# Optimization experiments

Hardware: AMD Instinct MI355X
Metric: run time of the kernel (lower is better)

## Reference

```python
import jax, jax.numpy as jnp
import numpy as np

EPS = 1e-5

def mean_std_norm(x):
    # instance norm without affine: per-(B,C) mean/std over spatial dims
    mean = jnp.mean(x, axis=(2, 3), keepdims=True)
    var = jnp.var(x, axis=(2, 3), keepdims=True)
    return (x - mean) / jnp.sqrt(var + EPS)

def conv1x1(x, w, b):
    # x: [B,C,H,W], w: [O,C], b: [O]
    return jnp.einsum('oc,bchw->bohw', w, x) + b[None, :, None, None]

def setup_inputs() -> dict:
    key = jax.random.key(0)
    ks = jax.random.split(key, 9)
    C = 512
    s = 1.0 / np.sqrt(C)
    inp = {
        'content_feat': jax.random.normal(ks[0], (4, C, 64, 64), dtype=jnp.float32),
        'f_w': jax.random.normal(ks[1], (C, C), dtype=jnp.float32) * s,
        'f_b': jnp.zeros((C,), dtype=jnp.float32),
        'g_w': jax.random.normal(ks[2], (C, C), dtype=jnp.float32) * s,
        'g_b': jnp.zeros((C,), dtype=jnp.float32),
        'h_w': jax.random.normal(ks[3], (C, C), dtype=jnp.float32) * s,
        'h_b': jnp.zeros((C,), dtype=jnp.float32),
        'o_w': jax.random.normal(ks[4], (C, C), dtype=jnp.float32) * s,
        'o_b': jnp.zeros((C,), dtype=jnp.float32),
    }
    return inp

def reference(content_feat, f_w, f_b, g_w, g_b, h_w, h_b, o_w, o_b):
    B, C, H, W = content_feat.shape
    HW = H * W
    norm = mean_std_norm(content_feat)
    # f(norm) -> [B, HW, C]; g(norm) -> [B, C, HW]
    F_Fc = conv1x1(norm, f_w, f_b).reshape(B, C, HW).transpose(0, 2, 1)
    G_Fs = conv1x1(norm, g_w, g_b).reshape(B, C, HW)
    energy = jnp.einsum('bnc,bcm->bnm', F_Fc, G_Fs)  # [B, HW, HW]
    attention = jax.nn.softmax(energy, axis=-1)
    H_Fs = conv1x1(content_feat, h_w, h_b).reshape(B, C, HW)
    # out = H_Fs @ attention^T : out[b,c,m] = sum_n H_Fs[b,c,n] * att[b,m,n]
    out = jnp.einsum('bcn,bmn->bcm', H_Fs, attention).reshape(B, C, H, W)
    out = conv1x1(out, o_w, o_b)
    return out + content_feat
```

## Files before the change

### kernel.cpp

```cpp
#include <hip/hip_runtime.h>


typedef __bf16 bf16_t;
typedef _Float16 f16_t;
typedef _Float16 f16x8 __attribute__((ext_vector_type(8)));
typedef float f32x4 __attribute__((ext_vector_type(4)));

#define LOG2E 1.44269504088896340736f

__device__ __forceinline__ void gload16(const void* g, void* l) {
  __builtin_amdgcn_global_load_lds(
      (const __attribute__((address_space(1))) void*)g,
      (__attribute__((address_space(3))) void*)l, 16, 0, 0);
}

__global__ void __launch_bounds__(256) stats_k(const float* __restrict__ x,
                                               float* __restrict__ mu,
                                               float* __restrict__ rs,
                                               f16_t* __restrict__ xv) {
  const int bc = blockIdx.x;
  const float4* row = (const float4*)(x + (size_t)bc * 4096);
  f16_t* vrow = xv + (size_t)bc * 4096;
  float s = 0.f, ss = 0.f;
  for (int i = threadIdx.x; i < 1024; i += 256) {
    float4 v = row[i];
    s += v.x + v.y + v.z + v.w;
    ss += v.x * v.x + v.y * v.y + v.z * v.z + v.w * v.w;
    alignas(8) f16_t h[4];
    h[0] = (f16_t)v.x; h[1] = (f16_t)v.y; h[2] = (f16_t)v.z; h[3] = (f16_t)v.w;
    *(uint2*)(vrow + i * 4) = *(const uint2*)h;
  }
#pragma unroll
  for (int o = 32; o >= 1; o >>= 1) {
    s += __shfl_down(s, o);
    ss += __shfl_down(ss, o);
  }
  __shared__ float as_[4], ass_[4];
  const int w = threadIdx.x >> 6;
  if ((threadIdx.x & 63) == 0) { as_[w] = s; ass_[w] = ss; }
  __syncthreads();
  if (threadIdx.x == 0) {
    float st = as_[0] + as_[1] + as_[2] + as_[3];
    float sst = ass_[0] + ass_[1] + ass_[2] + ass_[3];
    float m = st * (1.f / 4096.f);
    float var = sst * (1.f / 4096.f) - m * m;
    mu[bc] = m;
    rs[bc] = rsqrtf(var + 1e-5f);
  }
}

__global__ void __launch_bounds__(256) mt_k(const float* __restrict__ fw,
                                            const float* __restrict__ gw,
                                            f16_t* __restrict__ Mh) {
  __shared__ float Fs[32][64];
  __shared__ float Gs[32][64];
  const int t = threadIdx.x;
  const int it = blockIdx.x, jt = blockIdx.y;
  float acc[16];
#pragma unroll
  for (int i = 0; i < 16; ++i) acc[i] = 0.f;
  const int jl = t >> 2, ib = (t & 3) * 16;
  const int lr = t >> 4, lc4 = (t & 15) * 4;
  for (int cc = 0; cc < 16; ++cc) {
    __syncthreads();
#pragma unroll
    for (int rep = 0; rep < 2; ++rep) {
      const int r = lr + rep * 16;
      *(float4*)&Fs[r][lc4] = *(const float4*)(fw + (size_t)(cc * 32 + r) * 512 + it * 64 + lc4);
      *(float4*)&Gs[r][lc4] = *(const float4*)(gw + (size_t)(cc * 32 + r) * 512 + jt * 64 + lc4);
    }
    __syncthreads();
#pragma unroll
    for (int c = 0; c < 32; ++c) {
      const float gv = Gs[c][jl];
#pragma unroll
      for (int ii = 0; ii < 16; ++ii) acc[ii] += gv * Fs[c][ib + ii];
    }
  }
  alignas(16) f16_t hi[16];
#pragma unroll
  for (int ii = 0; ii < 16; ++ii) hi[ii] = (f16_t)acc[ii];
  const size_t o = (size_t)(jt * 64 + jl) * 512 + it * 64 + ib;
  *(uint4*)(Mh + o) = *(const uint4*)hi;
  *(uint4*)(Mh + o + 8) = *(const uint4*)(hi + 8);
}

__global__ void __launch_bounds__(256) mt2_k(const float* __restrict__ hw,
                                             const float* __restrict__ ow,
                                             f16_t* __restrict__ Wf) {
  __shared__ float Fs[32][64];
  __shared__ float Os[64][33];
  const int t = threadIdx.x;
  const int it = blockIdx.x, jt = blockIdx.y;
  float acc[16];
#pragma unroll
  for (int i = 0; i < 16; ++i) acc[i] = 0.f;
  const int jl = t >> 2, ib = (t & 3) * 16;
  const int lr = t >> 4, lc4 = (t & 15) * 4;
  const int oj = t >> 2, ok = (t & 3) * 8;
  for (int kc = 0; kc < 16; ++kc) {
    __syncthreads();
#pragma unroll
    for (int rep = 0; rep < 2; ++rep) {
      const int r = lr + rep * 16;
      *(float4*)&Fs[r][lc4] = *(const float4*)(hw + (size_t)(kc * 32 + r) * 512 + it * 64 + lc4);
    }
    {
      const float4 a = *(const float4*)(ow + (size_t)(jt * 64 + oj) * 512 + kc * 32 + ok);
      const float4 bq = *(const float4*)(ow + (size_t)(jt * 64 + oj) * 512 + kc * 32 + ok + 4);
      Os[oj][ok] = a.x; Os[oj][ok + 1] = a.y; Os[oj][ok + 2] = a.z; Os[oj][ok + 3] = a.w;
      Os[oj][ok + 4] = bq.x; Os[oj][ok + 5] = bq.y; Os[oj][ok + 6] = bq.z; Os[oj][ok + 7] = bq.w;
    }
    __syncthreads();
#pragma unroll
    for (int k = 0; k < 32; ++k) {
      const float gv = Os[jl][k];
#pragma unroll
      for (int ii = 0; ii < 16; ++ii) acc[ii] += gv * Fs[k][ib + ii];
    }
  }
  alignas(16) f16_t hi[16];
#pragma unroll
  for (int ii = 0; ii < 16; ++ii) hi[ii] = (f16_t)acc[ii];
  const size_t o = (size_t)(jt * 64 + jl) * 512 + it * 64 + ib;
  *(uint4*)(Wf + o) = *(const uint4*)hi;
  *(uint4*)(Wf + o + 8) = *(const uint4*)(hi + 8);
}

__global__ void __launch_bounds__(256) v_k(const float* __restrict__ gw,
                                           const float* __restrict__ fb,
                                           float* __restrict__ v) {
  const int j = blockIdx.x * 256 + threadIdx.x;
  float s = 0.f;
  for (int c = 0; c < 512; ++c) s += gw[(size_t)c * 512 + j] * fb[c];
  v[j] = s;
}

__global__ void __launch_bounds__(256) bias2_k(const float* __restrict__ ow,
                                               const float* __restrict__ hb,
                                               const float* __restrict__ ob,
                                               float* __restrict__ b2) {
  const int w = threadIdx.x >> 6, lane = threadIdx.x & 63;
  const int j = blockIdx.x * 4 + w;
  const float4 a = *(const float4*)(ow + (size_t)j * 512 + lane * 8);
  const float4 b = *(const float4*)(ow + (size_t)j * 512 + lane * 8 + 4);
  const float4 h0 = *(const float4*)(hb + lane * 8);
  const float4 h1 = *(const float4*)(hb + lane * 8 + 4);
  float s = a.x * h0.x + a.y * h0.y + a.z * h0.z + a.w * h0.w +
            b.x * h1.x + b.y * h1.y + b.z * h1.z + b.w * h1.w;
#pragma unroll
  for (int o2 = 32; o2 >= 1; o2 >>= 1) s += __shfl_down(s, o2);
  if (lane == 0) b2[j] = s + ob[j];
}

__global__ void __launch_bounds__(256) u_k(const float* __restrict__ v,
                                           const f16_t* __restrict__ xf,
                                           float* __restrict__ u) {
  const int w = threadIdx.x >> 6, lane = threadIdx.x & 63;
  const int m = blockIdx.x * 4 + w;
  const int b = blockIdx.y;
  const size_t o = ((size_t)b * 4096 + m) * 512 + lane * 8;
  const f16x8 vh = *(const f16x8*)(xf + o);
  const float4 v0 = *(const float4*)(v + lane * 8);
  const float4 v1 = *(const float4*)(v + lane * 8 + 4);
  float s = 0.f;
  const float* vp = &v0.x;
#pragma unroll
  for (int e = 0; e < 4; ++e) s += (float)vh[e] * vp[e];
  const float* vq = &v1.x;
#pragma unroll
  for (int e = 0; e < 4; ++e) s += (float)vh[4 + e] * vq[e];
#pragma unroll
  for (int o2 = 32; o2 >= 1; o2 >>= 1) s += __shfl_down(s, o2);
  if (lane == 0) u[(size_t)b * 4096 + m] = s;
}

__global__ void __launch_bounds__(256) normt_k(const float* __restrict__ x,
                                               const float* __restrict__ mu,
                                               const float* __restrict__ rs,
                                               f16_t* __restrict__ xf) {
  __shared__ float tile[64][65];
  const int t = threadIdx.x;
  const int nt = blockIdx.x, ct = blockIdx.y, b = blockIdx.z;
  const float* src = x + ((size_t)b * 512 + ct * 64) * 4096 + nt * 64;
  {
    const int r = t >> 4, cq = (t & 15) * 4;
#pragma unroll
    for (int it = 0; it < 4; ++it) {
      const int rr = r + it * 16;
      const float4 v = *(const float4*)(src + (size_t)rr * 4096 + cq);
      tile[rr][cq] = v.x; tile[rr][cq + 1] = v.y;
      tile[rr][cq + 2] = v.z; tile[rr][cq + 3] = v.w;
    }
  }
  __syncthreads();
  const int n = t & 63, ch = t >> 6;
  alignas(16) f16_t vf[16];
#pragma unroll
  for (int i = 0; i < 16; ++i) {
    const int c = ch * 16 + i;
    const float v = tile[c][n];
    const int gc = b * 512 + ct * 64 + c;
    vf[i] = (f16_t)((v - mu[gc]) * rs[gc]);
  }
  const size_t o = ((size_t)b * 4096 + nt * 64 + n) * 512 + ct * 64 + ch * 16;
  *(uint4*)(xf + o) = *(const uint4*)vf;
  *(uint4*)(xf + o + 8) = *(const uint4*)(vf + 8);
}

template <typename OT, int BIAS, bool RESID>
__global__ void __launch_bounds__(256) gemm_k(const f16_t* __restrict__ A,
                                              const f16_t* __restrict__ Bt,
                                              OT* __restrict__ C,
                                              const float* __restrict__ biasM,
                                              const float* __restrict__ biasN,
                                              const float* __restrict__ resid,
                                              long sAb, long sBb, long sCb, int ldC) {
  __shared__ alignas(16) f16_t As[2][128 * 64];
  __shared__ alignas(16) f16_t Bs[2][128 * 64];
  const int t = threadIdx.x;
  const int lane = t & 63;
  const int w = t >> 6;
  const int wr = w >> 1, wc = w & 1;
  const int l15 = lane & 15, lg = lane >> 4;
  const int b = blockIdx.z;
  const int m0 = blockIdx.y * 128, n0 = blockIdx.x * 128;
  const f16_t* Ab = A + (size_t)sAb * b + (size_t)m0 * 512;
  const f16_t* Bb = Bt + (size_t)sBb * b + (size_t)n0 * 512;
  const int srow = t >> 3;
  const int slot = t & 7;

  auto gstage = [&](int pb_, int ks_) {
#pragma unroll
    for (int r_ = 0; r_ < 4; ++r_) {
      const int rr_ = r_ * 32 + srow;
      const size_t go_ = (size_t)rr_ * 512 + ks_ * 64 + ((slot ^ (rr_ & 7)) * 8);
      gload16(Ab + go_, (char*)As[pb_] + r_ * 4096 + w * 1024);
      gload16(Bb + go_, (char*)Bs[pb_] + r_ * 4096 + w * 1024);
    }
  };

  const f32x4 z4 = {0.f, 0.f, 0.f, 0.f};
  f32x4 acc[4][4];
#pragma unroll
  for (int i = 0; i < 4; ++i)
#pragma unroll
    for (int j = 0; j < 4; ++j) acc[i][j] = z4;

  gstage(0, 0);
  __syncthreads();
  for (int ks = 0; ks < 8; ++ks) {
    const int pb = ks & 1;
    if (ks < 7) gstage(pb ^ 1, ks + 1);
#pragma unroll
    for (int kk = 0; kk < 2; ++kk) {
      f16x8 af[4], bfr[4];
#pragma unroll
      for (int i = 0; i < 4; ++i) {
        const int ra = wr * 64 + i * 16 + l15;
        af[i] = *(const f16x8*)((const char*)As[pb] + ra * 128 + (((kk * 4 + lg) ^ (ra & 7)) * 16));
        const int rb = wc * 64 + i * 16 + l15;
        bfr[i] = *(const f16x8*)((const char*)Bs[pb] + rb * 128 + (((kk * 4 + lg) ^ (rb & 7)) * 16));
      }
#pragma unroll
      for (int i = 0; i < 4; ++i)
#pragma unroll
        for (int j = 0; j < 4; ++j)
          acc[i][j] = __builtin_amdgcn_mfma_f32_16x16x32_f16(af[i], bfr[j], acc[i][j], 0, 0, 0);
    }
    __syncthreads();
  }
  OT* Cb = C + (size_t)sCb * b;
#pragma unroll
  for (int i = 0; i < 4; ++i) {
#pragma unroll
    for (int j = 0; j < 4; ++j) {
      const int n = n0 + wc * 64 + j * 16 + l15;
      float bn = 0.f;
      if (BIAS == 2) bn = biasN[n];
#pragma unroll
      for (int r = 0; r < 4; ++r) {
        const int m = m0 + wr * 64 + i * 16 + lg * 4 + r;
        float v = acc[i][j][r] + bn;
        if (BIAS == 1) v += biasM[m];
        if (RESID) v += resid[(size_t)sCb * b + (size_t)m * ldC + n];
        Cb[(size_t)m * ldC + n] = (OT)v;
      }
    }
  }
}

__global__ void __launch_bounds__(512, 1) flash_k(const f16_t* __restrict__ Z,
                                                  const f16_t* __restrict__ X,
                                                  const float* __restrict__ u,
                                                  const f16_t* __restrict__ Hv,
                                                  f16_t* __restrict__ Oat_t) {
  __shared__ alignas(16) f16_t K[2][64 * 256];
  __shared__ alignas(16) f16_t P[64 * 72];
  __shared__ float redm[4][2][16];
  __shared__ float reds[4][2][16];
  __shared__ float alds[64];
  __shared__ float llds[64];

  const int t = threadIdx.x;
  const int lane = t & 63;
  const int w = t >> 6;
  const int wq = w & 3, wk = w >> 2;
  const int l15 = lane & 15, lg = lane >> 4;
  const int bid = blockIdx.x;
  const int xcd = bid & 7;
  const int b = xcd >> 1;
  const int q0 = ((xcd & 1) * 32 + (bid >> 3)) * 64;

  const f16_t* Kb = X + (size_t)b * 4096 * 512;
  const f16_t* Vb = Hv + (size_t)b * 512 * 4096;
  const float* ub = u + (size_t)b * 4096;

  const int srow = w * 2 + (lane >> 5);
  const int slot32 = lane & 31;

  auto stagek = [&](int pb_, int kt_, int hf_) {
    const int k0_ = kt_ * 64;
#pragma unroll
    for (int r_ = 0; r_ < 4; ++r_) {
      const int row_ = r_ * 16 + srow;
      const size_t go_ = (size_t)(k0_ + row_) * 512 + hf_ * 256 + ((slot32 ^ (row_ & 7)) * 8);
      gload16(Kb + go_, (char*)K[pb_] + r_ * 8192 + w * 1024);
    }
  };

#define QKHALF(PB, HF)                                                                        \
  do {                                                                                        \
    _Pragma("unroll") for (int cwl_ = 0; cwl_ < 8; ++cwl_) {                                  \
      const f16x8 qf_ = qf[(HF) * 8 + cwl_];                                                  \
      _Pragma("unroll") for (int mf_ = 0; mf_ < 2; ++mf_) {                                   \
        const int key_ = 32 * wk + 16 * mf_ + l15;                                            \
        const int so_ = ((cwl_ * 4 + lg) ^ (key_ & 7)) * 16;                                  \
        const f16x8 kf_ = *(const f16x8*)((const char*)K[PB] + key_ * 512 + so_);             \
        sacc[mf_] = __builtin_amdgcn_mfma_f32_16x16x32_f16(kf_, qf_, sacc[mf_], 0, 0, 0);     \
      }                                                                                       \
    }                                                                                         \
  } while (0)

  f16x8 qf[16];
  {
    const size_t qo = ((size_t)b * 4096 + q0 + 16 * wq + l15) * 512 + lg * 8;
#pragma unroll
    for (int cw = 0; cw < 16; ++cw) qf[cw] = *(const f16x8*)(Z + qo + cw * 32);
  }
  stagek(0, 0, 0);

  const f32x4 z4 = {0.f, 0.f, 0.f, 0.f};
  f32x4 oacc[4][4];
#pragma unroll
  for (int i = 0; i < 4; ++i)
#pragma unroll
    for (int j = 0; j < 4; ++j) oacc[i][j] = z4;
  float m_run = -3.0e38f, l_run = 0.f;
  const int qrow = 16 * wq + l15;

  __syncthreads();

  for (int kt = 0; kt < 64; ++kt) {
    const int k0 = kt * 64;
    f32x4 sacc[2] = {z4, z4};
    const float4 u0 = *(const float4*)(ub + k0 + 32 * wk + 4 * lg);
    const float4 u1 = *(const float4*)(ub + k0 + 32 * wk + 16 + 4 * lg);
    stagek(1, kt, 1);
    QKHALF(0, 0);
    __syncthreads();
    if (kt < 63) stagek(0, kt + 1, 0);
    f16x8 vpre[4][2];
#pragma unroll
    for (int ct = 0; ct < 4; ++ct) {
      const int c = 64 * w + 16 * ct + l15;
#pragma unroll
      for (int kk = 0; kk < 2; ++kk)
        vpre[ct][kk] = *(const f16x8*)(Vb + (size_t)c * 4096 + k0 + kk * 32 + lg * 8);
    }
    QKHALF(1, 1);
    float pm = -3.0e38f;
    {
      const float* up0 = &u0.x;
      const float* up1 = &u1.x;
#pragma unroll
      for (int j = 0; j < 4; ++j) {
        sacc[0][j] += up0[j];
        sacc[1][j] += up1[j];
        pm = fmaxf(pm, fmaxf(sacc[0][j], sacc[1][j]));
      }
    }
    pm = fmaxf(pm, __shfl_xor(pm, 16));
    pm = fmaxf(pm, __shfl_xor(pm, 32));
    if (lane < 16) redm[wq][wk][lane] = pm;
    __syncthreads();
    const float m_tile = fmaxf(pm, redm[wq][wk ^ 1][l15]);
    float alpha;
    if (m_tile > m_run + 8.f) {
      alpha = exp2f((m_run - m_tile) * LOG2E);
      m_run = m_tile;
    } else {
      alpha = 1.f;
    }
    float ps = 0.f;
    {
      alignas(8) f16_t pk[4];
#pragma unroll
      for (int mf = 0; mf < 2; ++mf) {
#pragma unroll
        for (int j = 0; j < 4; ++j) {
          const float p = exp2f((sacc[mf][j] - m_run) * LOG2E);
          ps += p;
          pk[j] = (f16_t)p;
        }
        *(uint2*)((char*)P + qrow * 144 + 64 * wk + 32 * mf + 8 * lg) = *(const uint2*)pk;
      }
    }
    ps += __shfl_xor(ps, 16);
    ps += __shfl_xor(ps, 32);
    if (lane < 16) {
      reds[wq][wk][lane] = ps;
      if (wk == 0) alds[16 * wq + lane] = alpha;
    }
    __syncthreads();
    const float s_tile = reds[wq][0][l15] + reds[wq][1][l15];
    l_run = l_run * alpha + s_tile;
    float aq[4];
#pragma unroll
    for (int qt = 0; qt < 4; ++qt) aq[qt] = alds[16 * qt + l15];
    const bool need = (aq[0] != 1.f) || (aq[1] != 1.f) || (aq[2] != 1.f) || (aq[3] != 1.f);
    if (__any(need)) {
#pragma unroll
      for (int ct = 0; ct < 4; ++ct)
#pragma unroll
        for (int qt = 0; qt < 4; ++qt) oacc[ct][qt] *= aq[qt];
    }
#pragma unroll
    for (int kk = 0; kk < 2; ++kk) {
      f16x8 bp[4];
#pragma unroll
      for (int qt = 0; qt < 4; ++qt) {
        const int q = 16 * qt + l15;
        bp[qt] = *(const f16x8*)((const char*)P + q * 144 + kk * 64 + lg * 16);
      }
#pragma unroll
      for (int ct = 0; ct < 4; ++ct)
#pragma unroll
        for (int qt = 0; qt < 4; ++qt)
          oacc[ct][qt] =
              __builtin_amdgcn_mfma_f32_16x16x32_f16(vpre[ct][kk], bp[qt], oacc[ct][qt], 0, 0, 0);
    }
  }
#undef QKHALF
  if (wk == 0 && lane < 16) llds[16 * wq + lane] = l_run;
  __syncthreads();
  float inv[4];
#pragma unroll
  for (int qt = 0; qt < 4; ++qt) inv[qt] = 1.f / llds[16 * qt + l15];
#pragma unroll
  for (int ct = 0; ct < 4; ++ct)
#pragma unroll
    for (int qt = 0; qt < 4; ++qt) {
      alignas(8) f16_t o4[4];
#pragma unroll
      for (int j = 0; j < 4; ++j) o4[j] = (f16_t)(oacc[ct][qt][j] * inv[qt]);
      *(uint2*)(Oat_t + ((size_t)b * 4096 + q0 + 16 * qt + l15) * 512 + 64 * w + 16 * ct + 4 * lg) =
          *(const uint2*)o4;
    }
}

extern "C" void kernel_launch(void* const* d_in, const int* in_sizes, int n_in,
                              void* d_out, int out_size, void* d_ws, size_t ws_size,
                              hipStream_t stream) {
  const float* x = (const float*)d_in[0];
  const float* fw = (const float*)d_in[1];
  const float* fb = (const float*)d_in[2];
  const float* gw = (const float*)d_in[3];
  const float* gb = (const float*)d_in[4];
  const float* hw = (const float*)d_in[5];
  const float* hb = (const float*)d_in[6];
  const float* ow = (const float*)d_in[7];
  const float* ob = (const float*)d_in[8];
  float* out = (float*)d_out;
  (void)gb;

  const size_t BIG = (size_t)4 * 4096 * 512 * sizeof(f16_t);
  char* p = (char*)d_ws;
  float* mu = (float*)p; p += 2048 * sizeof(float);
  float* rs = (float*)p; p += 2048 * sizeof(float);
  float* vv = (float*)p; p += 512 * sizeof(float);
  float* b2 = (float*)p; p += 512 * sizeof(float);
  float* uu = (float*)p; p += (size_t)4 * 4096 * sizeof(float);
  f16_t* Mh = (f16_t*)p; p += (size_t)512 * 512 * sizeof(f16_t);
  f16_t* Wf = (f16_t*)p; p += (size_t)512 * 512 * sizeof(f16_t);
  f16_t* xf = (f16_t*)p; p += BIG;
  f16_t* xv = (f16_t*)p; p += BIG;
  f16_t* Zf = (f16_t*)p; p += BIG;
  f16_t* Oat_t = (f16_t*)p; p += BIG;

  const long sD = (long)4096 * 512;

  stats_k<<<2048, 256, 0, stream>>>(x, mu, rs, xv);
  mt_k<<<dim3(8, 8), 256, 0, stream>>>(fw, gw, Mh);
  mt2_k<<<dim3(8, 8), 256, 0, stream>>>(hw, ow, Wf);
  v_k<<<2, 256, 0, stream>>>(gw, fb, vv);
  bias2_k<<<128, 256, 0, stream>>>(ow, hb, ob, b2);
  normt_k<<<dim3(64, 8, 4), 256, 0, stream>>>(x, mu, rs, xf);
  u_k<<<dim3(1024, 4), 256, 0, stream>>>(vv, xf, uu);
  gemm_k<f16_t, 0, false><<<dim3(4, 32, 4), 256, 0, stream>>>(
      xf, Mh, Zf, nullptr, nullptr, nullptr, sD, 0, sD, 512);
  flash_k<<<256, 512, 0, stream>>>(Zf, xf, uu, xv, Oat_t);
  gemm_k<float, 1, true><<<dim3(32, 4, 4), 256, 0, stream>>>(
      Wf, Oat_t, out, b2, nullptr, x, 0, sD, sD, 4096);

  (void)in_sizes; (void)n_in; (void)out_size; (void)ws_size;
}
```

Measured before the change: 389.7 us.

## Merge weight-prep kernels into one launch and split QK MFMA accumulator chains

Four small weight-preprocessing kernels (two weight products and two bias vectors) are combined into a single launch, with blocks dispatching by index, to cut launch overhead. The bias2 computation changes from a wave-per-row shuffle reduction to a serial per-thread loop over strided rows. Separately, the QK score loop in the flash kernel now alternates between two independent accumulator sets per key fragment to shorten MFMA dependency chains. The extra accumulators raise register pressure in the flash kernel.

```diff
diff --git a/kernel.cpp b/kernel.cpp
--- a/kernel.cpp
+++ b/kernel.cpp
@@ -49,13 +49,11 @@
   }
 }
 
-__global__ void __launch_bounds__(256) mt_k(const float* __restrict__ fw,
-                                            const float* __restrict__ gw,
-                                            f16_t* __restrict__ Mh) {
-  __shared__ float Fs[32][64];
-  __shared__ float Gs[32][64];
+__device__ void mt_body(const float* __restrict__ A, const float* __restrict__ B,
+                        f16_t* __restrict__ Out, int it, int jt, float* sm, bool bIsJK) {
+  float* Fs = sm;
+  float* Gs = sm + 2048;
   const int t = threadIdx.x;
-  const int it = blockIdx.x, jt = blockIdx.y;
   float acc[16];
 #pragma unroll
   for (int i = 0; i < 16; ++i) acc[i] = 0.f;
@@ -66,91 +64,63 @@
 #pragma unroll
     for (int rep = 0; rep < 2; ++rep) {
       const int r = lr + rep * 16;
-      *(float4*)&Fs[r][lc4] = *(const float4*)(fw + (size_t)(cc * 32 + r) * 512 + it * 64 + lc4);
-      *(float4*)&Gs[r][lc4] = *(const float4*)(gw + (size_t)(cc * 32 + r) * 512 + jt * 64 + lc4);
+      *(float4*)&Fs[r * 64 + lc4] = *(const float4*)(A + (size_t)(cc * 32 + r) * 512 + it * 64 + lc4);
+      if (!bIsJK)
+        *(float4*)&Gs[r * 64 + lc4] = *(const float4*)(B + (size_t)(cc * 32 + r) * 512 + jt * 64 + lc4);
+    }
+    if (bIsJK) {
+      const int oj = t >> 2, ok = (t & 3) * 8;
+      const float4 a = *(const float4*)(B + (size_t)(jt * 64 + oj) * 512 + cc * 32 + ok);
+      const float4 bq = *(const float4*)(B + (size_t)(jt * 64 + oj) * 512 + cc * 32 + ok + 4);
+      Gs[oj * 33 + ok] = a.x; Gs[oj * 33 + ok + 1] = a.y;
+      Gs[oj * 33 + ok + 2] = a.z; Gs[oj * 33 + ok + 3] = a.w;
+      Gs[oj * 33 + ok + 4] = bq.x; Gs[oj * 33 + ok + 5] = bq.y;
+      Gs[oj * 33 + ok + 6] = bq.z; Gs[oj * 33 + ok + 7] = bq.w;
     }
     __syncthreads();
 #pragma unroll
     for (int c = 0; c < 32; ++c) {
-      const float gv = Gs[c][jl];
-#pragma unroll
-      for (int ii = 0; ii < 16; ++ii) acc[ii] += gv * Fs[c][ib + ii];
+      const float gv = bIsJK ? Gs[jl * 33 + c] : Gs[c * 64 + jl];
+#pragma unroll
+      for (int ii = 0; ii < 16; ++ii) acc[ii] += gv * Fs[c * 64 + ib + ii];
     }
   }
   alignas(16) f16_t hi[16];
 #pragma unroll
   for (int ii = 0; ii < 16; ++ii) hi[ii] = (f16_t)acc[ii];
   const size_t o = (size_t)(jt * 64 + jl) * 512 + it * 64 + ib;
-  *(uint4*)(Mh + o) = *(const uint4*)hi;
-  *(uint4*)(Mh + o + 8) = *(const uint4*)(hi + 8);
-}
-
-__global__ void __launch_bounds__(256) mt2_k(const float* __restrict__ hw,
-                                             const float* __restrict__ ow,
-                                             f16_t* __restrict__ Wf) {
-  __shared__ float Fs[32][64];
-  __shared__ float Os[64][33];
-  const int t = threadIdx.x;
-  const int it = blockIdx.x, jt = blockIdx.y;
-  float acc[16];
-#pragma unroll
-  for (int i = 0; i < 16; ++i) acc[i] = 0.f;
-  const int jl = t >> 2, ib = (t & 3) * 16;
-  const int lr = t >> 4, lc4 = (t & 15) * 4;
-  const int oj = t >> 2, ok = (t & 3) * 8;
-  for (int kc = 0; kc < 16; ++kc) {
-    __syncthreads();
-#pragma unroll
-    for (int rep = 0; rep < 2; ++rep) {
-      const int r = lr + rep * 16;
-      *(float4*)&Fs[r][lc4] = *(const float4*)(hw + (size_t)(kc * 32 + r) * 512 + it * 64 + lc4);
-    }
-    {
-      const float4 a = *(const float4*)(ow + (size_t)(jt * 64 + oj) * 512 + kc * 32 + ok);
-      const float4 bq = *(const float4*)(ow + (size_t)(jt * 64 + oj) * 512 + kc * 32 + ok + 4);
-      Os[oj][ok] = a.x; Os[oj][ok + 1] = a.y; Os[oj][ok + 2] = a.z; Os[oj][ok + 3] = a.w;
-      Os[oj][ok + 4] = bq.x; Os[oj][ok + 5] = bq.y; Os[oj][ok + 6] = bq.z; Os[oj][ok + 7] = bq.w;
-    }
-    __syncthreads();
-#pragma unroll
-    for (int k = 0; k < 32; ++k) {
-      const float gv = Os[jl][k];
-#pragma unroll
-      for (int ii = 0; ii < 16; ++ii) acc[ii] += gv * Fs[k][ib + ii];
-    }
-  }
-  alignas(16) f16_t hi[16];
-#pragma unroll
-  for (int ii = 0; ii < 16; ++ii) hi[ii] = (f16_t)acc[ii];
-  const size_t o = (size_t)(jt * 64 + jl) * 512 + it * 64 + ib;
-  *(uint4*)(Wf + o) = *(const uint4*)hi;
-  *(uint4*)(Wf + o + 8) = *(const uint4*)(hi + 8);
-}
-
-__global__ void __launch_bounds__(256) v_k(const float* __restrict__ gw,
-                                           const float* __restrict__ fb,
-                                           float* __restrict__ v) {
-  const int j = blockIdx.x * 256 + threadIdx.x;
-  float s = 0.f;
-  for (int c = 0; c < 512; ++c) s += gw[(size_t)c * 512 + j] * fb[c];
-  v[j] = s;
-}
-
-__global__ void __launch_bounds__(256) bias2_k(const float* __restrict__ ow,
-                                               const float* __restrict__ hb,
-                                               const float* __restrict__ ob,
-                                               float* __restrict__ b2) {
-  const int w = threadIdx.x >> 6, lane = threadIdx.x & 63;
-  const int j = blockIdx.x * 4 + w;
-  const float4 a = *(const float4*)(ow + (size_t)j * 512 + lane * 8);
-  const float4 b = *(const float4*)(ow + (size_t)j * 512 + lane * 8 + 4);
-  const float4 h0 = *(const float4*)(hb + lane * 8);
-  const float4 h1 = *(const float4*)(hb + lane * 8 + 4);
-  float s = a.x * h0.x + a.y * h0.y + a.z * h0.z + a.w * h0.w +
-            b.x * h1.x + b.y * h1.y + b.z * h1.z + b.w * h1.w;
-#pragma unroll
-  for (int o2 = 32; o2 >= 1; o2 >>= 1) s += __shfl_down(s, o2);
-  if (lane == 0) b2[j] = s + ob[j];
+  *(uint4*)(Out + o) = *(const uint4*)hi;
+  *(uint4*)(Out + o + 8) = *(const uint4*)(hi + 8);
+}
+
+__global__ void __launch_bounds__(256) prep_k(const float* __restrict__ fw,
+                                              const float* __restrict__ gw,
+                                              const float* __restrict__ hw,
+                                              const float* __restrict__ ow,
+                                              const float* __restrict__ fb,
+                                              const float* __restrict__ hb,
+                                              const float* __restrict__ ob,
+                                              f16_t* __restrict__ Mh,
+                                              f16_t* __restrict__ Wf,
+                                              float* __restrict__ vv,
+                                              float* __restrict__ b2) {
+  __shared__ float sm[2048 + 64 * 33];
+  const int bb = blockIdx.x;
+  if (bb < 64) {
+    mt_body(fw, gw, Mh, bb & 7, bb >> 3, sm, false);
+  } else if (bb < 128) {
+    mt_body(hw, ow, Wf, (bb - 64) & 7, (bb - 64) >> 3, sm, true);
+  } else if (bb < 130) {
+    const int j = (bb - 128) * 256 + threadIdx.x;
+    float s = 0.f;
+    for (int c = 0; c < 512; ++c) s += gw[(size_t)c * 512 + j] * fb[c];
+    vv[j] = s;
+  } else {
+    const int j = (bb - 130) * 256 + threadIdx.x;
+    float s = 0.f;
+    for (int c = 0; c < 512; ++c) s += ow[(size_t)j * 512 + c] * hb[c];
+    b2[j] = s + ob[j];
+  }
 }
 
 __global__ void __launch_bounds__(256) u_k(const float* __restrict__ v,
@@ -331,15 +301,25 @@
 
 #define QKHALF(PB, HF)                                                                        \
   do {                                                                                        \
+    f32x4 e0 = z4, e1 = z4, d0 = z4, d1 = z4;                                                 \
     _Pragma("unroll") for (int cwl_ = 0; cwl_ < 8; ++cwl_) {                                  \
       const f16x8 qf_ = qf[(HF) * 8 + cwl_];                                                  \
-      _Pragma("unroll") for (int mf_ = 0; mf_ < 2; ++mf_) {                                   \
-        const int key_ = 32 * wk + 16 * mf_ + l15;                                            \
-        const int so_ = ((cwl_ * 4 + lg) ^ (key_ & 7)) * 16;                                  \
-        const f16x8 kf_ = *(const f16x8*)((const char*)K[PB] + key_ * 512 + so_);             \
-        sacc[mf_] = __builtin_amdgcn_mfma_f32_16x16x32_f16(kf_, qf_, sacc[mf_], 0, 0, 0);     \
+      const int key0_ = 32 * wk + l15;                                                        \
+      const int key1_ = 32 * wk + 16 + l15;                                                   \
+      const f16x8 kf0_ = *(const f16x8*)((const char*)K[PB] + key0_ * 512 +                   \
+                                         (((cwl_ * 4 + lg) ^ (key0_ & 7)) * 16));             \
+      const f16x8 kf1_ = *(const f16x8*)((const char*)K[PB] + key1_ * 512 +                   \
+                                         (((cwl_ * 4 + lg) ^ (key1_ & 7)) * 16));             \
+      if (cwl_ & 1) {                                                                         \
+        d0 = __builtin_amdgcn_mfma_f32_16x16x32_f16(kf0_, qf_, d0, 0, 0, 0);                  \
+        d1 = __builtin_amdgcn_mfma_f32_16x16x32_f16(kf1_, qf_, d1, 0, 0, 0);                  \
+      } else {                                                                                \
+        e0 = __builtin_amdgcn_mfma_f32_16x16x32_f16(kf0_, qf_, e0, 0, 0, 0);                  \
+        e1 = __builtin_amdgcn_mfma_f32_16x16x32_f16(kf1_, qf_, e1, 0, 0, 0);                  \
       }                                                                                       \
     }                                                                                         \
+    sacc[0] += e0 + d0;                                                                       \
+    sacc[1] += e1 + d1;                                                                       \
   } while (0)
 
   f16x8 qf[16];
@@ -501,10 +481,7 @@
   const long sD = (long)4096 * 512;
 
   stats_k<<<2048, 256, 0, stream>>>(x, mu, rs, xv);
-  mt_k<<<dim3(8, 8), 256, 0, stream>>>(fw, gw, Mh);
-  mt2_k<<<dim3(8, 8), 256, 0, stream>>>(hw, ow, Wf);
-  v_k<<<2, 256, 0, stream>>>(gw, fb, vv);
-  bias2_k<<<128, 256, 0, stream>>>(ow, hb, ob, b2);
+  prep_k<<<132, 256, 0, stream>>>(fw, gw, hw, ow, fb, hb, ob, Mh, Wf, vv, b2);
   normt_k<<<dim3(64, 8, 4), 256, 0, stream>>>(x, mu, rs, xf);
   u_k<<<dim3(1024, 4), 256, 0, stream>>>(vv, xf, uu);
   gemm_k<f16_t, 0, false><<<dim3(4, 32, 4), 256, 0, stream>>>(
```

Result: no change. 392.3 us (+0.7%).
